# Optimization experiments

Measured on AMD Instinct MI355X. Metric: run time of the kernel, lower is better.

## Reference

```python
import jax, jax.numpy as jnp
import numpy as np

N, H, W = 2, 96, 96
HL, WL = 48, 48
NCLS = 59


def _bn_params(key, c):
    k1, k2, k3, k4 = jax.random.split(key, 4)
    g = jax.random.uniform(k1, (c,), minval=0.5, maxval=1.5)
    b = jax.random.normal(k2, (c,)) * 0.1
    m = jax.random.normal(k3, (c,)) * 0.1
    v = jax.random.uniform(k4, (c,), minval=0.5, maxval=1.5)
    return jnp.stack([g, b, m, v])  # [4, C]


def _conv_w(key, shape):
    fan_in = shape[1] * shape[2] * shape[3]
    return jax.random.normal(key, shape) / np.sqrt(fan_in)


def setup_inputs() -> dict:
    key = jax.random.key(0)
    ks = jax.random.split(key, 32)
    return {
        "c1": jax.random.normal(ks[0], (N, 256, H, W)),
        "c2": jax.random.normal(ks[1], (N, 512, HL, WL)),
        "x": jax.random.normal(ks[2], (N, 2048, HL, WL)),
        "w_r1": _conv_w(ks[3], (64, 256, 3, 3)), "bn_r1": _bn_params(ks[4], 64),
        "w_r2": _conv_w(ks[5], (64, 64, 3, 3)), "bn_r2": _bn_params(ks[6], 64),
        "w_r3": _conv_w(ks[7], (64, 512, 1, 1)), "bn_r3": _bn_params(ks[8], 64),
        "w_p1": _conv_w(ks[9], (512, 2048, 1, 1)), "bn_p1": _bn_params(ks[10], 512),
        "w_p2": _conv_w(ks[11], (512, 2048, 1, 1)), "bn_p2": _bn_params(ks[12], 512),
        "w_p3": _conv_w(ks[13], (512, 2048, 1, 1)), "bn_p3": _bn_params(ks[14], 512),
        "w_p4": _conv_w(ks[15], (512, 2048, 1, 1)), "bn_p4": _bn_params(ks[16], 512),
        "w_c5": _conv_w(ks[17], (512, 4096, 3, 3)), "bn_c5": _bn_params(ks[18], 512),
        "w_c6": _conv_w(ks[19], (NCLS, 512, 1, 1)),
        "b_c6": jax.random.normal(ks[20], (NCLS,)) * 0.01,
    }


def conv2d(x, w, padding=0, dilation=1):
    return jax.lax.conv_general_dilated(
        x, w, window_strides=(1, 1), padding=[(padding, padding)] * 2,
        rhs_dilation=(dilation, dilation),
        dimension_numbers=("NCHW", "OIHW", "NCHW"))


def bn(x, p, eps=1e-5):
    g, b, m, v = p[0], p[1], p[2], p[3]
    scale = g * jax.lax.rsqrt(v + eps)
    return (x - m[None, :, None, None]) * scale[None, :, None, None] + b[None, :, None, None]


def resize_bilinear_ac(x, oh, ow):
    # bilinear, align_corners=True (matches torch interpolate)
    n, c, h, w = x.shape
    def coords(inp, out):
        if inp == 1 or out == 1:
            return jnp.zeros((out,), jnp.float32)
        return jnp.arange(out, dtype=jnp.float32) * ((inp - 1) / (out - 1))
    ys, xs = coords(h, oh), coords(w, ow)
    y0 = jnp.clip(jnp.floor(ys).astype(jnp.int32), 0, h - 1)
    y1 = jnp.clip(y0 + 1, 0, h - 1)
    wy = (ys - y0)[None, None, :, None]
    x0 = jnp.clip(jnp.floor(xs).astype(jnp.int32), 0, w - 1)
    x1 = jnp.clip(x0 + 1, 0, w - 1)
    wx = (xs - x0)[None, None, :]
    g = x[:, :, y0, :] * (1.0 - wy) + x[:, :, y1, :] * wy  # [n,c,oh,w]
    return g[:, :, :, x0] * (1.0 - wx[:, None]) + g[:, :, :, x1] * wx[:, None]


def unfold3x3_d2(x):
    # torch unfold(kernel=3, dilation=2, padding=2, stride=1) -> [n,c,9,h*w]
    n, c, h, w = x.shape
    p = jnp.pad(x, ((0, 0), (0, 0), (2, 2), (2, 2)))
    pats = jnp.stack([p[:, :, dy:dy + h, dx:dx + w]
                      for dy in (0, 2, 4) for dx in (0, 2, 4)], axis=2)
    return pats.reshape(n, c, 9, h * w)


def adaptive_avg_pool(x, s):
    n, c, h, w = x.shape  # h, w divisible by s here
    return x.reshape(n, c, s, h // s, s, w // s).mean(axis=(3, 5))


def reference(c1, c2, x, w_r1, bn_r1, w_r2, bn_r2, w_r3, bn_r3,
              w_p1, bn_p1, w_p2, bn_p2, w_p3, bn_p3, w_p4, bn_p4,
              w_c5, bn_c5, w_c6, b_c6):
    n, _, h, w = c1.shape
    # refine(c1): two dilated 3x3 convs -> query features [n,64,h,w]
    r = jax.nn.relu(bn(conv2d(c1, w_r1, padding=2, dilation=2), bn_r1))
    r = jax.nn.relu(bn(conv2d(r, w_r2, padding=2, dilation=2), bn_r2))
    # c2 -> upsample -> refine2 (1x1) -> key features [n,64,h,w]
    c2u = resize_bilinear_ac(c2, h, w)
    c2r = jax.nn.relu(bn(conv2d(c2u, w_r3), bn_r3))
    uc2 = unfold3x3_d2(c2r)                       # [n,64,9,hw]
    q = r.reshape(n, 64, h * w)                   # [n,64,hw]
    energy = jnp.einsum("ncp,nckp->npk", q, uc2)  # [n,hw,9]
    att = jax.nn.softmax(energy, axis=-1)
    # conv5 = PyramidPooling + 3x3 conv(4096->512) + BN + ReLU
    xh, xw = x.shape[2], x.shape[3]
    feats = [x]
    for s, wp, bnp in ((1, w_p1, bn_p1), (2, w_p2, bn_p2), (3, w_p3, bn_p3), (6, w_p4, bn_p4)):
        p = jax.nn.relu(bn(conv2d(adaptive_avg_pool(x, s), wp), bnp))
        feats.append(resize_bilinear_ac(p, xh, xw))
    psp = jnp.concatenate(feats, axis=1)          # [n,4096,xh,xw]
    out = jax.nn.relu(bn(conv2d(psp, w_c5, padding=1, dilation=1), bn_c5))  # [n,512,xh,xw]
    out0 = resize_bilinear_ac(out, h, w)          # [n,512,h,w]
    uo = unfold3x3_d2(out0)                       # [n,512,9,hw]
    agg = jnp.einsum("npk,nckp->ncp", att, uo).reshape(n, 512, h, w)
    # conv6: Dropout2d in eval mode = identity, then 1x1 conv with bias
    return conv2d(agg, w_c6) + b_c6[None, :, None, None]
```

## Files before the change

### kernel.cpp

```cpp
#include <hip/hip_runtime.h>
#include <hip/hip_bf16.h>
#include <cstddef>
#include <cstdint>

typedef __hip_bfloat16 hbf;
typedef __bf16 bf16x8 __attribute__((ext_vector_type(8)));
typedef float f32x4 __attribute__((ext_vector_type(4)));

#define GLDS(gp, lp) __builtin_amdgcn_global_load_lds( \
    (const __attribute__((address_space(1))) void*)(gp), \
    (__attribute__((address_space(3))) void*)(lp), 16, 0, 0)

__device__ __forceinline__ void bn_coef(const float* __restrict__ p, int C, int c,
                                        float& s, float& t) {
    float g = p[c];
    float b = p[C + c];
    float m = p[2 * C + c];
    float v = p[3 * C + c];
    s = g * rsqrtf(v + 1e-5f);
    t = b - m * s;
}

__global__ void k_fill0(uint32_t* __restrict__ p, int n) {
    int i = blockIdx.x * blockDim.x + threadIdx.x;
    if (i < n) p[i] = 0u;
}

__global__ __launch_bounds__(256) void k_c1trans(const float* __restrict__ x,
                                                 hbf* __restrict__ c1t) {
    __shared__ float tbuf[32][33];
    const int p0 = blockIdx.x * 32, c0 = blockIdx.y * 32, n = blockIdx.z;
    const int tx = threadIdx.x, ty = threadIdx.y;
#pragma unroll
    for (int i = 0; i < 4; ++i) {
        int ci = c0 + ty * 4 + i;
        tbuf[ty * 4 + i][tx] = x[((size_t)(n * 256 + ci)) * 9216 + p0 + tx];
    }
    __syncthreads();
#pragma unroll
    for (int i = 0; i < 4; ++i) {
        int p = p0 + ty * 4 + i;
        int pp = (p / 96 + 2) * 100 + (p % 96) + 2;
        c1t[((size_t)(n * 10000 + pp)) * 256 + c0 + tx] = __float2bfloat16(tbuf[tx][ty * 4 + i]);
    }
}

template <int CI>
__global__ __launch_bounds__(256) void k_wtrans_small(const float* __restrict__ w,
                                                      hbf* __restrict__ wt) {
    int idx = blockIdx.x * 256 + threadIdx.x;
    int co = idx / CI, ci = idx % CI;
    const float* s = w + ((size_t)(co * CI + ci)) * 9;
#pragma unroll
    for (int tap = 0; tap < 9; ++tap)
        wt[((size_t)(tap * 64 + co)) * CI + ci] = __float2bfloat16(s[tap]);
}

template <int CI>
__global__ __launch_bounds__(256) void k_dconv_mfma(const hbf* __restrict__ wt,
                                                    const hbf* __restrict__ it,
                                                    float* __restrict__ accout) {
    __shared__ hbf As[3][64 * 32];
    __shared__ hbf Bs[72 * 32];
    const int tid = threadIdx.x;
    const int l = tid & 63, w = tid >> 6;
    const int P0 = blockIdx.x * 64;
    const int g  = blockIdx.y;
    const int r0 = tid >> 2;
    const int swzk = ((tid & 3) ^ (r0 & 3)) * 8;

    const int n_i = P0 / 9216;
    const int pl0 = P0 - n_i * 9216;
    const int pp0 = (pl0 / 96 + 2) * 100 + (pl0 % 96) + 2;
    const ptrdiff_t browbase = (ptrdiff_t)n_i * 10000 + pp0 + (g - 1) * 200 - 2;

    const int wn = w * 16;
    const int pl_lane = pl0 + wn + (l & 15);
    const int jb = ((pl_lane / 96 + 2) * 100 + (pl_lane % 96) + 2) - pp0;
    const int slotA = ((l >> 4) ^ (l & 3)) * 8;

    f32x4 acc[4];
#pragma unroll
    for (int i = 0; i < 4; ++i) acc[i] = {0.f, 0.f, 0.f, 0.f};

    const hbf* gA = wt + ((size_t)(g * 192 + r0)) * CI + swzk;
    const hbf* gB = it + (size_t)(browbase + r0) * CI + swzk;
    hbf* ldsA = (hbf*)As[0] + w * 512;
    hbf* ldsB = Bs + w * 512;

    for (int k0 = 0; k0 < CI; k0 += 32) {
        __syncthreads();
#pragma unroll
        for (int t = 0; t < 3; ++t)
            GLDS(gA + (size_t)t * 64 * CI + k0, ldsA + t * 2048);
        GLDS(gB + k0, ldsB);
        if (tid < 32)
            GLDS(gB + (size_t)64 * CI + k0, Bs + 2048);
        __syncthreads();
#pragma unroll
        for (int t = 0; t < 3; ++t) {
            const int brow = jb + 2 * t;
            bf16x8 bfr = *(const bf16x8*)(Bs + brow * 32 + (((l >> 4) ^ (brow & 3)) * 8));
#pragma unroll
            for (int ti = 0; ti < 4; ++ti) {
                bf16x8 af = *(const bf16x8*)(&As[t][(ti * 16 + (l & 15)) * 32 + slotA]);
                acc[ti] = __builtin_amdgcn_mfma_f32_16x16x32_bf16(af, bfr, acc[ti], 0, 0, 0);
            }
        }
    }
    const int px = P0 + wn + (l & 15);
    const int n2 = px / 9216, pl2 = px % 9216;
#pragma unroll
    for (int ti = 0; ti < 4; ++ti) {
        const int mrow = ti * 16 + (l >> 4) * 4;
        float* dst = accout + ((size_t)(n2 * 64 + mrow)) * 9216 + pl2;
#pragma unroll
        for (int r = 0; r < 4; ++r)
            atomicAdd(dst + (size_t)r * 9216, acc[ti][r]);
    }
}

__global__ __launch_bounds__(256) void k_ep_r1(const float* __restrict__ acc,
                                               const float* __restrict__ bnp,
                                               hbf* __restrict__ r1t) {
    __shared__ float ss[64], st[64];
    if (threadIdx.x < 64) {
        float s, t; bn_coef(bnp, 64, threadIdx.x, s, t);
        ss[threadIdx.x] = s; st[threadIdx.x] = t;
    }
    __syncthreads();
    const int pi = blockIdx.x * 256 + threadIdx.x;
    const int n = pi / 9216, pl = pi % 9216;
    const int pp = (pl / 96 + 2) * 100 + (pl % 96) + 2;
    hbf* dst = r1t + ((size_t)(n * 10000 + pp)) * 64;
    const float* src = acc + (size_t)n * 64 * 9216 + pl;
#pragma unroll
    for (int co = 0; co < 64; ++co)
        dst[co] = __float2bfloat16(fmaxf(fmaf(src[(size_t)co * 9216], ss[co], st[co]), 0.f));
}

__global__ void k_ep_q(const float* __restrict__ acc, const float* __restrict__ bnp,
                       float* __restrict__ q) {
    int idx = blockIdx.x * blockDim.x + threadIdx.x;
    int c = (idx / 9216) & 63;
    float s, t; bn_coef(bnp, 64, c, s, t);
    q[idx] = fmaxf(fmaf(acc[idx], s, t), 0.f);
}

__global__ __launch_bounds__(192) void k_conv1x1_c2(const float* __restrict__ c2,
                                                    const float* __restrict__ w,
                                                    float* __restrict__ outacc) {
    const int x = threadIdx.x;
    const int y = blockIdx.y * 4 + threadIdx.y;
    const int n = blockIdx.z >> 2;
    const int ci0 = (blockIdx.z & 3) * 128;
    const int cg = blockIdx.x;
    const int p = y * 48 + x;
    float acc[4];
#pragma unroll
    for (int j = 0; j < 4; ++j) acc[j] = 0.f;
    for (int ci = ci0; ci < ci0 + 128; ++ci) {
        float iv = c2[(size_t)(n * 512 + ci) * 2304 + p];
#pragma unroll
        for (int j = 0; j < 4; ++j)
            acc[j] = fmaf(iv, w[(size_t)(cg * 4 + j) * 512 + ci], acc[j]);
    }
#pragma unroll
    for (int j = 0; j < 4; ++j)
        atomicAdd(&outacc[(size_t)(n * 64 + cg * 4 + j) * 2304 + p], acc[j]);
}

__global__ void k_up96(const float* __restrict__ src, float* __restrict__ dst,
                       int C, const float* __restrict__ bnp) {
    int idx = blockIdx.x * blockDim.x + threadIdx.x;
    int p = idx % 9216;
    int nc = idx / 9216;
    int c = nc % C;
    int y = p / 96, x = p % 96;
    int yn = y * 47, xn = x * 47;
    int y0 = yn / 95, x0 = xn / 95;
    float wy = (float)(yn - y0 * 95) * (1.f / 95.f);
    float wx = (float)(xn - x0 * 95) * (1.f / 95.f);
    int y1 = min(y0 + 1, 47), x1 = min(x0 + 1, 47);
    const float* sp = src + (size_t)nc * 2304;
    float v00 = sp[y0 * 48 + x0], v01 = sp[y0 * 48 + x1];
    float v10 = sp[y1 * 48 + x0], v11 = sp[y1 * 48 + x1];
    float v = (v00 * (1.f - wx) + v01 * wx) * (1.f - wy)
            + (v10 * (1.f - wx) + v11 * wx) * wy;
    if (bnp) {
        float s, t; bn_coef(bnp, C, c, s, t);
        v = fmaxf(fmaf(v, s, t), 0.f);
    }
    dst[idx] = v;
}

__global__ __launch_bounds__(128) void k_attention(const float* __restrict__ q,
                                                   const float* __restrict__ kf,
                                                   float* __restrict__ att) {
    int tid = blockIdx.x * 128 + threadIdx.x;
    int n = tid / 9216, p = tid % 9216;
    int y = p / 96, x = p % 96;
    float qv[64];
    const float* qb = q + (size_t)n * 64 * 9216 + p;
#pragma unroll
    for (int c = 0; c < 64; ++c) qv[c] = qb[(size_t)c * 9216];
    float e[9];
    const float* kb = kf + (size_t)n * 64 * 9216;
#pragma unroll
    for (int ky = 0; ky < 3; ++ky)
#pragma unroll
        for (int kx = 0; kx < 3; ++kx) {
            int yy = y + 2 * ky - 2, xx = x + 2 * kx - 2;
            float s = 0.f;
            if (yy >= 0 && yy < 96 && xx >= 0 && xx < 96) {
                const float* kp = kb + yy * 96 + xx;
#pragma unroll
                for (int c = 0; c < 64; ++c) s = fmaf(qv[c], kp[(size_t)c * 9216], s);
            }
            e[ky * 3 + kx] = s;
        }
    float m = e[0];
#pragma unroll
    for (int k = 1; k < 9; ++k) m = fmaxf(m, e[k]);
    float sum = 0.f;
#pragma unroll
    for (int k = 0; k < 9; ++k) { e[k] = __expf(e[k] - m); sum += e[k]; }
    float inv = 1.f / sum;
    float* ap = att + (size_t)tid * 9;
#pragma unroll
    for (int k = 0; k < 9; ++k) ap[k] = e[k] * inv;
}

__global__ __launch_bounds__(64) void k_pool(const float* __restrict__ xin,
                                             float* __restrict__ pooled) {
    int b = blockIdx.x;
    int t = threadIdx.x;
    __shared__ float cells[50];
    if (t < 50) cells[t] = 0.f;
    __syncthreads();
    float rs = 0.f;
    if (t < 48) {
        const float* row = xin + (size_t)b * 2304 + t * 48;
        float s6[6];
#pragma unroll
        for (int j = 0; j < 6; ++j) {
            float s = 0.f;
#pragma unroll
            for (int i = 0; i < 8; ++i) s += row[j * 8 + i];
            s6[j] = s;
        }
        float s3a = s6[0] + s6[1], s3b = s6[2] + s6[3], s3c = s6[4] + s6[5];
        float s2a = s3a + s6[2], s2b = s6[3] + s3c;
        rs = s2a + s2b;
        int r6 = t >> 3, r3 = t >> 4, r2 = t / 24;
        atomicAdd(&cells[14 + r6 * 6 + 0], s6[0]);
        atomicAdd(&cells[14 + r6 * 6 + 1], s6[1]);
        atomicAdd(&cells[14 + r6 * 6 + 2], s6[2]);
        atomicAdd(&cells[14 + r6 * 6 + 3], s6[3]);
        atomicAdd(&cells[14 + r6 * 6 + 4], s6[4]);
        atomicAdd(&cells[14 + r6 * 6 + 5], s6[5]);
        atomicAdd(&cells[5 + r3 * 3 + 0], s3a);
        atomicAdd(&cells[5 + r3 * 3 + 1], s3b);
        atomicAdd(&cells[5 + r3 * 3 + 2], s3c);
        atomicAdd(&cells[1 + r2 * 2 + 0], s2a);
        atomicAdd(&cells[1 + r2 * 2 + 1], s2b);
    }
#pragma unroll
    for (int off = 32; off > 0; off >>= 1) rs += __shfl_down(rs, off);
    if (t == 0) atomicAdd(&cells[0], rs);
    __syncthreads();
    if (t < 50) {
        float inv = (t == 0) ? (1.f / 2304.f)
                  : (t < 5)  ? (1.f / 576.f)
                  : (t < 14) ? (1.f / 256.f)
                             : (1.f / 64.f);
        pooled[(size_t)b * 50 + t] = cells[t] * inv;
    }
}

__global__ __launch_bounds__(64) void k_pconv2(const float* __restrict__ pooled,
        const float* __restrict__ wp1, const float* __restrict__ bn1,
        const float* __restrict__ wp2, const float* __restrict__ bn2,
        const float* __restrict__ wp3, const float* __restrict__ bn3,
        const float* __restrict__ wp4, const float* __restrict__ bn4,
        float* __restrict__ pconv) {
    const int co = blockIdx.x, n = blockIdx.y;
    const int t = threadIdx.x;
    const int cell = (t < 50) ? t : 49;
    const float* w; const float* bnp;
    if (cell == 0)      { w = wp1; bnp = bn1; }
    else if (cell < 5)  { w = wp2; bnp = bn2; }
    else if (cell < 14) { w = wp3; bnp = bn3; }
    else                { w = wp4; bnp = bn4; }
    const float* pin = pooled + (size_t)n * 2048 * 50 + cell;
    const float* wr = w + (size_t)co * 2048;
    float a0 = 0.f, a1 = 0.f, a2 = 0.f, a3 = 0.f;
    for (int c = 0; c < 2048; c += 4) {
        a0 = fmaf(pin[(size_t)c * 50],       wr[c],     a0);
        a1 = fmaf(pin[(size_t)(c + 1) * 50], wr[c + 1], a1);
        a2 = fmaf(pin[(size_t)(c + 2) * 50], wr[c + 2], a2);
        a3 = fmaf(pin[(size_t)(c + 3) * 50], wr[c + 3], a3);
    }
    float a = (a0 + a1) + (a2 + a3);
    float s, tt; bn_coef(bnp, 512, co, s, tt);
    if (t < 50)
        pconv[((size_t)n * 512 + co) * 50 + cell] = fmaxf(fmaf(a, s, tt), 0.f);
}

__global__ __launch_bounds__(256) void k_wpsp_trans(const float* __restrict__ w5,
                                                    hbf* __restrict__ wpsp) {
    const int co = blockIdx.x * 64 + (threadIdx.x & 63);
    const int b = blockIdx.y;
    const int c0 = blockIdx.z * 64 + (threadIdx.x >> 6) * 16;
    for (int i = 0; i < 16; ++i) {
        int c = c0 + i;
        const float* s = w5 + ((size_t)co * 4096 + 2048 + b * 512 + c) * 9;
#pragma unroll
        for (int tap = 0; tap < 9; ++tap)
            wpsp[(((size_t)(tap * 4 + b) * 512) + c) * 512 + co] = __float2bfloat16(s[tap]);
    }
}

__global__ __launch_bounds__(64) void k_computeM2(const hbf* __restrict__ wpsp,
                                                  const float* __restrict__ pconv,
                                                  float* __restrict__ M) {
    const int cog = blockIdx.x, tap = blockIdx.y;
    const int n = blockIdx.z / 7, chunk = blockIdx.z % 7;
    const int cell0_t[7] = {0, 1, 5, 14, 23, 32, 41};
    const int ncell_t[7] = {1, 4, 9, 9, 9, 9, 9};
    const int btab[7]    = {0, 1, 2, 3, 3, 3, 3};
    const int cell0 = cell0_t[chunk], nc = ncell_t[chunk], b = btab[chunk];
    const int co = cog * 64 + threadIdx.x;
    const hbf* wb = wpsp + ((size_t)(tap * 4 + b) * 512) * 512 + co;
    const float* pc = pconv + (size_t)n * 512 * 50 + cell0;
    float acc[9];
#pragma unroll
    for (int j = 0; j < 9; ++j) acc[j] = 0.f;
    for (int c = 0; c < 512; ++c) {
        float w = __bfloat162float(wb[(size_t)c * 512]);
#pragma unroll
        for (int j = 0; j < 9; ++j)
            acc[j] = fmaf(w, pc[c * 50 + j], acc[j]);
    }
    float* Mp = M + ((size_t)(n * 512 + co) * 9 + tap) * 50 + cell0;
    for (int j = 0; j < nc; ++j) Mp[j] = acc[j];
}

struct B4 { int c0, c1, c2, c3; float w0, w1, w2, w3; };
__device__ __forceinline__ B4 cell_interp(int yy, int xx, int s, int base) {
    int sm1 = s - 1;
    int yn = yy * sm1, xn = xx * sm1;
    int y0 = yn / 47, x0 = xn / 47;
    float wy = (float)(yn - y0 * 47) * (1.f / 47.f);
    float wx = (float)(xn - x0 * 47) * (1.f / 47.f);
    int y1 = min(y0 + 1, sm1), x1 = min(x0 + 1, sm1);
    B4 r;
    r.c0 = base + y0 * s + x0; r.c1 = base + y0 * s + x1;
    r.c2 = base + y1 * s + x0; r.c3 = base + y1 * s + x1;
    r.w0 = (1.f - wy) * (1.f - wx); r.w1 = (1.f - wy) * wx;
    r.w2 = wy * (1.f - wx);         r.w3 = wy * wx;
    return r;
}

__global__ __launch_bounds__(256) void k_xtrans(const float* __restrict__ x,
                                                hbf* __restrict__ xtp) {
    __shared__ float tbuf[32][33];
    const int p0 = blockIdx.x * 32, c0 = blockIdx.y * 32, n = blockIdx.z;
    const int tx = threadIdx.x, ty = threadIdx.y;
#pragma unroll
    for (int i = 0; i < 4; ++i) {
        int ci = c0 + ty * 4 + i;
        tbuf[ty * 4 + i][tx] = x[((size_t)(n * 2048 + ci)) * 2304 + p0 + tx];
    }
    __syncthreads();
#pragma unroll
    for (int i = 0; i < 4; ++i) {
        int p = p0 + ty * 4 + i;
        int pp = (p / 48 + 1) * 50 + (p % 48) + 1;
        xtp[((size_t)(n * 2500 + pp)) * 2048 + c0 + tx] = __float2bfloat16(tbuf[tx][ty * 4 + i]);
    }
}

__global__ __launch_bounds__(256) void k_wtrans(const float* __restrict__ w5,
                                                hbf* __restrict__ wt) {
    int idx = blockIdx.x * 256 + threadIdx.x;
    int co = idx >> 11, ci = idx & 2047;
    const float* s = w5 + ((size_t)co * 4096 + ci) * 9;
#pragma unroll
    for (int tap = 0; tap < 9; ++tap)
        wt[((size_t)(tap * 512 + co)) * 2048 + ci] = __float2bfloat16(s[tap]);
}

__global__ __launch_bounds__(256) void k_conv5_mfma(const hbf* __restrict__ wt,
                                                    const hbf* __restrict__ xtp,
                                                    float* __restrict__ c5acc) {
    __shared__ hbf As[3][128 * 32];
    __shared__ hbf Bs[136 * 32];
    const int tid = threadIdx.x;
    const int l = tid & 63, w = tid >> 6;
    const int m0 = blockIdx.x * 128;
    const int P0 = blockIdx.y * 128;
    const int g  = blockIdx.z >> 1;
    const int kh = blockIdx.z & 1;
    const int n_img = P0 / 2304;
    const int pbase = P0 - n_img * 2304;
    const int r0 = tid >> 2;
    const int swzk = ((tid & 3) ^ (r0 & 3)) * 8;

    const int pp0 = pbase + 2 * (pbase / 48) + 51;
    const ptrdiff_t browbase = (ptrdiff_t)n_img * 2500 + pp0 + (g - 1) * 50 - 1;

    const int wm = (w & 1) * 64, wn = (w >> 1) * 64;
    int jb[4];
#pragma unroll
    for (int tj = 0; tj < 4; ++tj) {
        int p = pbase + wn + tj * 16 + (l & 15);
        jb[tj] = p + 2 * (p / 48) + 51 - pp0;
    }
    const int slotA = ((l >> 4) ^ (l & 3)) * 8;

    f32x4 acc[4][4];
#pragma unroll
    for (int i = 0; i < 4; ++i)
#pragma unroll
        for (int j = 0; j < 4; ++j) acc[i][j] = {0.f, 0.f, 0.f, 0.f};

    const int kbase = kh * 1024;
    const hbf* gA = wt + ((size_t)(g * 1536 + m0 + r0)) * 2048 + kbase + swzk;
    const hbf* gB = xtp + (size_t)(browbase + r0) * 2048 + kbase + swzk;
    hbf* ldsA = (hbf*)As[0] + w * 512;
    hbf* ldsB = Bs + w * 512;

    for (int k0 = 0; k0 < 1024; k0 += 32) {
        __syncthreads();
#pragma unroll
        for (int t = 0; t < 3; ++t) {
            GLDS(gA + (size_t)t * 512 * 2048 + k0,             ldsA + t * 4096);
            GLDS(gA + (size_t)t * 512 * 2048 + 64 * 2048 + k0, ldsA + t * 4096 + 2048);
        }
        GLDS(gB + k0,                      ldsB);
        GLDS(gB + (size_t)64 * 2048 + k0,  ldsB + 2048);
        if (tid < 32)
            GLDS(gB + (size_t)128 * 2048 + k0, Bs + 4096);
        __syncthreads();
#pragma unroll
        for (int t = 0; t < 3; ++t) {
            bf16x8 af[4], bfr[4];
#pragma unroll
            for (int ti = 0; ti < 4; ++ti)
                af[ti] = *(const bf16x8*)(&As[t][(wm + ti * 16 + (l & 15)) * 32 + slotA]);
#pragma unroll
            for (int tj = 0; tj < 4; ++tj) {
                const int brow = jb[tj] + t;
                bfr[tj] = *(const bf16x8*)(Bs + brow * 32 + (((l >> 4) ^ (brow & 3)) * 8));
            }
#pragma unroll
            for (int ti = 0; ti < 4; ++ti)
#pragma unroll
                for (int tj = 0; tj < 4; ++tj)
                    acc[ti][tj] = __builtin_amdgcn_mfma_f32_16x16x32_bf16(
                        af[ti], bfr[tj], acc[ti][tj], 0, 0, 0);
        }
    }
#pragma unroll
    for (int ti = 0; ti < 4; ++ti) {
        const int mrow = wm + ti * 16 + (l >> 4) * 4;
#pragma unroll
        for (int tj = 0; tj < 4; ++tj) {
            const int p = pbase + wn + tj * 16 + (l & 15);
            float* dst = c5acc + ((size_t)(n_img * 512 + m0 + mrow)) * 2304 + p;
#pragma unroll
            for (int r = 0; r < 4; ++r)
                atomicAdd(dst + (size_t)r * 2304, acc[ti][tj][r]);
        }
    }
}

__global__ __launch_bounds__(256) void k_bnrelu_psp(const float* __restrict__ c5acc,
                                                    const float* __restrict__ M,
                                                    const float* __restrict__ bnp,
                                                    hbf* __restrict__ c5out) {
    const int co = blockIdx.x, n = blockIdx.y;
    __shared__ float Ms[450];
    const float* Mrow = M + ((size_t)(n * 512 + co)) * 450;
    for (int i = threadIdx.x; i < 450; i += 256) Ms[i] = Mrow[i];
    __syncthreads();
    float s, t; bn_coef(bnp, 512, co, s, t);
    const size_t base = ((size_t)(n * 512 + co)) * 2304;
#pragma unroll
    for (int i = 0; i < 9; ++i) {
        int p = threadIdx.x + i * 256;
        int y = p / 48, x = p % 48;
        float a = c5acc[base + p];
#pragma unroll
        for (int ky = 0; ky < 3; ++ky) {
            int yy = y + ky - 1;
            if (yy < 0 || yy > 47) continue;
#pragma unroll
            for (int kx = 0; kx < 3; ++kx) {
                int xx = x + kx - 1;
                if (xx < 0 || xx > 47) continue;
                const float* Mp = Ms + (ky * 3 + kx) * 50;
                float sa = Mp[0];
                B4 b2 = cell_interp(yy, xx, 2, 1);
                B4 b3 = cell_interp(yy, xx, 3, 5);
                B4 b6 = cell_interp(yy, xx, 6, 14);
                sa = fmaf(b2.w0, Mp[b2.c0], sa); sa = fmaf(b2.w1, Mp[b2.c1], sa);
                sa = fmaf(b2.w2, Mp[b2.c2], sa); sa = fmaf(b2.w3, Mp[b2.c3], sa);
                sa = fmaf(b3.w0, Mp[b3.c0], sa); sa = fmaf(b3.w1, Mp[b3.c1], sa);
                sa = fmaf(b3.w2, Mp[b3.c2], sa); sa = fmaf(b3.w3, Mp[b3.c3], sa);
                sa = fmaf(b6.w0, Mp[b6.c0], sa); sa = fmaf(b6.w1, Mp[b6.c1], sa);
                sa = fmaf(b6.w2, Mp[b6.c2], sa); sa = fmaf(b6.w3, Mp[b6.c3], sa);
                a += sa;
            }
        }
        c5out[base + p] = __float2bfloat16(fmaxf(fmaf(a, s, t), 0.f));
    }
}

__global__ __launch_bounds__(192) void k_conv6s(const hbf* __restrict__ c5o,
                                                const float* __restrict__ w,
                                                float* __restrict__ out) {
    const int x = threadIdx.x;
    const int y = blockIdx.y * 4 + threadIdx.y;
    const int n = blockIdx.z;
    const int co = blockIdx.x;
    const int p = y * 48 + x;
    const hbf* ip = c5o + (size_t)n * 512 * 2304 + p;
    const float* wr = w + (size_t)co * 512;
    float a0 = 0.f, a1 = 0.f, a2 = 0.f, a3 = 0.f;
    for (int ci = 0; ci < 512; ci += 4) {
        a0 = fmaf(__bfloat162float(ip[(size_t)ci * 2304]),       wr[ci],     a0);
        a1 = fmaf(__bfloat162float(ip[(size_t)(ci + 1) * 2304]), wr[ci + 1], a1);
        a2 = fmaf(__bfloat162float(ip[(size_t)(ci + 2) * 2304]), wr[ci + 2], a2);
        a3 = fmaf(__bfloat162float(ip[(size_t)(ci + 3) * 2304]), wr[ci + 3], a3);
    }
    out[((size_t)n * 59 + co) * 2304 + p] = (a0 + a1) + (a2 + a3);
}

__global__ void k_final(const float* __restrict__ att, const float* __restrict__ c6o,
                        const float* __restrict__ bias, float* __restrict__ out) {
    int idx = blockIdx.x * blockDim.x + threadIdx.x;
    int p = idx % 9216;
    int nc = idx / 9216;
    int cls = nc % 59, n = nc / 59;
    int y = p / 96, x = p % 96;
    const float* ar = att + ((size_t)n * 9216 + p) * 9;
    const float* cp = c6o + (size_t)nc * 9216;
    float a = bias[cls];
#pragma unroll
    for (int ky = 0; ky < 3; ++ky)
#pragma unroll
        for (int kx = 0; kx < 3; ++kx) {
            int yy = y + 2 * ky - 2, xx = x + 2 * kx - 2;
            if (yy >= 0 && yy < 96 && xx >= 0 && xx < 96)
                a = fmaf(ar[ky * 3 + kx], cp[yy * 96 + xx], a);
        }
    out[idx] = a;
}

extern "C" void kernel_launch(void* const* d_in, const int* in_sizes, int n_in,
                              void* d_out, int out_size, void* d_ws, size_t ws_size,
                              hipStream_t stream) {
    const float* c1    = (const float*)d_in[0];
    const float* c2    = (const float*)d_in[1];
    const float* xin   = (const float*)d_in[2];
    const float* w_r1  = (const float*)d_in[3];
    const float* bn_r1 = (const float*)d_in[4];
    const float* w_r2  = (const float*)d_in[5];
    const float* bn_r2 = (const float*)d_in[6];
    const float* w_r3  = (const float*)d_in[7];
    const float* bn_r3 = (const float*)d_in[8];
    const float* w_p1  = (const float*)d_in[9];
    const float* bn_p1 = (const float*)d_in[10];
    const float* w_p2  = (const float*)d_in[11];
    const float* bn_p2 = (const float*)d_in[12];
    const float* w_p3  = (const float*)d_in[13];
    const float* bn_p3 = (const float*)d_in[14];
    const float* w_p4  = (const float*)d_in[15];
    const float* bn_p4 = (const float*)d_in[16];
    const float* w_c5  = (const float*)d_in[17];
    const float* bn_c5 = (const float*)d_in[18];
    const float* w_c6  = (const float*)d_in[19];
    const float* b_c6  = (const float*)d_in[20];
    float* out = (float*)d_out;
    (void)in_sizes; (void)n_in; (void)out_size; (void)ws_size;

    char* base = (char*)d_ws;
    float* att = (float*)base;
    char*  A   = base + 663552;
    hbf*   c1t   = (hbf*)A;
    hbf*   r1t   = (hbf*)(A + 10240000);
    float* r1acc = (float*)(A + 12800000);
    float* qacc  = (float*)(A + 17518592);
    float* c2acc = (float*)(A + 22237184);
    float* q     = (float*)(A + 23416832);
    float* c2r   = (float*)(A + 28135424);
    hbf*   wr1t  = (hbf*)(A + 32854016);
    hbf*   wr2t  = (hbf*)(A + 33148928);
    hbf*   wpsp   = (hbf*)A;
    float* pooled = (float*)(A + 48791552);
    float* pconv  = (float*)(A + 49610752);
    float* M      = (float*)(A + 49815552);
    hbf*   xtp    = (hbf*)A;
    float* c5acc  = (float*)(A + 20480000);
    hbf*   wt     = (hbf*)(A + 29917184);
    hbf*   c5out = (hbf*)A;
    float* c6s   = (float*)(A + 4718592);
    float* c6o   = (float*)(A + 5806080);

    k_fill0<<<dim3(22868), 256, 0, stream>>>((uint32_t*)A, 5854208);
    k_c1trans<<<dim3(288, 8, 2), dim3(32, 8), 0, stream>>>(c1, c1t);
    k_wtrans_small<256><<<dim3(64), 256, 0, stream>>>(w_r1, wr1t);
    k_wtrans_small<64><<<dim3(16), 256, 0, stream>>>(w_r2, wr2t);
    k_dconv_mfma<256><<<dim3(288, 3), 256, 0, stream>>>(wr1t, c1t, r1acc);
    k_ep_r1<<<dim3(72), 256, 0, stream>>>(r1acc, bn_r1, r1t);
    k_dconv_mfma<64><<<dim3(288, 3), 256, 0, stream>>>(wr2t, r1t, qacc);
    k_ep_q<<<dim3(4608), 256, 0, stream>>>(qacc, bn_r2, q);
    k_conv1x1_c2<<<dim3(16, 12, 8), dim3(48, 4), 0, stream>>>(c2, w_r3, c2acc);
    k_up96<<<dim3(2 * 64 * 9216 / 256), 256, 0, stream>>>(c2acc, c2r, 64, bn_r3);
    k_attention<<<dim3(144), 128, 0, stream>>>(q, c2r, att);
    k_pool<<<dim3(4096), 64, 0, stream>>>(xin, pooled);
    k_pconv2<<<dim3(512, 2), 64, 0, stream>>>(pooled, w_p1, bn_p1, w_p2, bn_p2,
                                              w_p3, bn_p3, w_p4, bn_p4, pconv);
    k_wpsp_trans<<<dim3(8, 4, 8), 256, 0, stream>>>(w_c5, wpsp);
    k_computeM2<<<dim3(8, 9, 14), 64, 0, stream>>>(wpsp, pconv, M);
    k_fill0<<<dim3(29216), 256, 0, stream>>>((uint32_t*)xtp, 7479296);
    k_xtrans<<<dim3(72, 64, 2), dim3(32, 8), 0, stream>>>(xin, xtp);
    k_wtrans<<<dim3(4096), 256, 0, stream>>>(w_c5, wt);
    k_conv5_mfma<<<dim3(4, 36, 6), 256, 0, stream>>>(wt, xtp, c5acc);
    k_bnrelu_psp<<<dim3(512, 2), 256, 0, stream>>>(c5acc, M, bn_c5, c5out);
    k_conv6s<<<dim3(59, 12, 2), dim3(48, 4), 0, stream>>>(c5out, w_c6, c6s);
    k_up96<<<dim3(2 * 59 * 9216 / 256), 256, 0, stream>>>(c6s, c6o, 59, nullptr);
    k_final<<<dim3(2 * 59 * 9216 / 256), 256, 0, stream>>>(att, c6o, b_c6, out);
}
```

Baseline: 791.5 us.

## Double-buffer LDS staging in MFMA convs and drop conv5 K-split

```diff
diff --git a/kernel.cpp b/kernel.cpp
--- a/kernel.cpp
+++ b/kernel.cpp
@@ -60,8 +60,8 @@
 __global__ __launch_bounds__(256) void k_dconv_mfma(const hbf* __restrict__ wt,
                                                     const hbf* __restrict__ it,
                                                     float* __restrict__ accout) {
-    __shared__ hbf As[3][64 * 32];
-    __shared__ hbf Bs[72 * 32];
+    __shared__ hbf As[2][3][64 * 32];
+    __shared__ hbf Bs[2][72 * 32];
     const int tid = threadIdx.x;
     const int l = tid & 63, w = tid >> 6;
     const int P0 = blockIdx.x * 64;
@@ -85,29 +85,39 @@
 
     const hbf* gA = wt + ((size_t)(g * 192 + r0)) * CI + swzk;
     const hbf* gB = it + (size_t)(browbase + r0) * CI + swzk;
-    hbf* ldsA = (hbf*)As[0] + w * 512;
-    hbf* ldsB = Bs + w * 512;
-
+
+#define STAGE_D(buf, k0) do {                                                  \
+        hbf* ldsA_ = &As[buf][0][0] + w * 512;                                 \
+        hbf* ldsB_ = &Bs[buf][0] + w * 512;                                    \
+        _Pragma("unroll")                                                      \
+        for (int t_ = 0; t_ < 3; ++t_)                                         \
+            GLDS(gA + (size_t)t_ * 64 * CI + (k0), ldsA_ + t_ * 2048);         \
+        GLDS(gB + (k0), ldsB_);                                                \
+        if (tid < 32)                                                          \
+            GLDS(gB + (size_t)64 * CI + (k0), &Bs[buf][0] + 2048);             \
+    } while (0)
+
+    STAGE_D(0, 0);
+    __syncthreads();
+    int cur = 0;
+#pragma unroll 2
     for (int k0 = 0; k0 < CI; k0 += 32) {
-        __syncthreads();
-#pragma unroll
-        for (int t = 0; t < 3; ++t)
-            GLDS(gA + (size_t)t * 64 * CI + k0, ldsA + t * 2048);
-        GLDS(gB + k0, ldsB);
-        if (tid < 32)
-            GLDS(gB + (size_t)64 * CI + k0, Bs + 2048);
-        __syncthreads();
+        if (k0 + 32 < CI) STAGE_D(cur ^ 1, k0 + 32);
 #pragma unroll
         for (int t = 0; t < 3; ++t) {
             const int brow = jb + 2 * t;
-            bf16x8 bfr = *(const bf16x8*)(Bs + brow * 32 + (((l >> 4) ^ (brow & 3)) * 8));
+            bf16x8 bfr = *(const bf16x8*)(&Bs[cur][0] + brow * 32 + (((l >> 4) ^ (brow & 3)) * 8));
 #pragma unroll
             for (int ti = 0; ti < 4; ++ti) {
-                bf16x8 af = *(const bf16x8*)(&As[t][(ti * 16 + (l & 15)) * 32 + slotA]);
+                bf16x8 af = *(const bf16x8*)(&As[cur][t][(ti * 16 + (l & 15)) * 32 + slotA]);
                 acc[ti] = __builtin_amdgcn_mfma_f32_16x16x32_bf16(af, bfr, acc[ti], 0, 0, 0);
             }
         }
-    }
+        __syncthreads();
+        cur ^= 1;
+    }
+#undef STAGE_D
+
     const int px = P0 + wn + (l & 15);
     const int n2 = px / 9216, pl2 = px % 9216;
 #pragma unroll
@@ -394,14 +404,13 @@
 __global__ __launch_bounds__(256) void k_conv5_mfma(const hbf* __restrict__ wt,
                                                     const hbf* __restrict__ xtp,
                                                     float* __restrict__ c5acc) {
-    __shared__ hbf As[3][128 * 32];
-    __shared__ hbf Bs[136 * 32];
+    __shared__ hbf As[2][3][128 * 32];
+    __shared__ hbf Bs[2][136 * 32];
     const int tid = threadIdx.x;
     const int l = tid & 63, w = tid >> 6;
     const int m0 = blockIdx.x * 128;
     const int P0 = blockIdx.y * 128;
-    const int g  = blockIdx.z >> 1;
-    const int kh = blockIdx.z & 1;
+    const int g  = blockIdx.z;
     const int n_img = P0 / 2304;
     const int pbase = P0 - n_img * 2304;
     const int r0 = tid >> 2;
@@ -425,34 +434,39 @@
 #pragma unroll
         for (int j = 0; j < 4; ++j) acc[i][j] = {0.f, 0.f, 0.f, 0.f};
 
-    const int kbase = kh * 1024;
-    const hbf* gA = wt + ((size_t)(g * 1536 + m0 + r0)) * 2048 + kbase + swzk;
-    const hbf* gB = xtp + (size_t)(browbase + r0) * 2048 + kbase + swzk;
-    hbf* ldsA = (hbf*)As[0] + w * 512;
-    hbf* ldsB = Bs + w * 512;
-
-    for (int k0 = 0; k0 < 1024; k0 += 32) {
-        __syncthreads();
-#pragma unroll
-        for (int t = 0; t < 3; ++t) {
-            GLDS(gA + (size_t)t * 512 * 2048 + k0,             ldsA + t * 4096);
-            GLDS(gA + (size_t)t * 512 * 2048 + 64 * 2048 + k0, ldsA + t * 4096 + 2048);
-        }
-        GLDS(gB + k0,                      ldsB);
-        GLDS(gB + (size_t)64 * 2048 + k0,  ldsB + 2048);
-        if (tid < 32)
-            GLDS(gB + (size_t)128 * 2048 + k0, Bs + 4096);
-        __syncthreads();
+    const hbf* gA = wt + ((size_t)(g * 1536 + m0 + r0)) * 2048 + swzk;
+    const hbf* gB = xtp + (size_t)(browbase + r0) * 2048 + swzk;
+
+#define STAGE5(buf, k0) do {                                                       \
+        hbf* ldsA_ = &As[buf][0][0] + w * 512;                                     \
+        hbf* ldsB_ = &Bs[buf][0] + w * 512;                                        \
+        _Pragma("unroll")                                                          \
+        for (int t_ = 0; t_ < 3; ++t_) {                                           \
+            GLDS(gA + (size_t)t_ * 512 * 2048 + (k0),             ldsA_ + t_ * 4096);      \
+            GLDS(gA + (size_t)t_ * 512 * 2048 + 64 * 2048 + (k0), ldsA_ + t_ * 4096 + 2048); \
+        }                                                                          \
+        GLDS(gB + (k0),                      ldsB_);                               \
+        GLDS(gB + (size_t)64 * 2048 + (k0),  ldsB_ + 2048);                        \
+        if (tid < 32)                                                              \
+            GLDS(gB + (size_t)128 * 2048 + (k0), &Bs[buf][0] + 4096);              \
+    } while (0)
+
+    STAGE5(0, 0);
+    __syncthreads();
+    int cur = 0;
+#pragma unroll 2
+    for (int k0 = 0; k0 < 2048; k0 += 32) {
+        if (k0 + 32 < 2048) STAGE5(cur ^ 1, k0 + 32);
 #pragma unroll
         for (int t = 0; t < 3; ++t) {
             bf16x8 af[4], bfr[4];
 #pragma unroll
             for (int ti = 0; ti < 4; ++ti)
-                af[ti] = *(const bf16x8*)(&As[t][(wm + ti * 16 + (l & 15)) * 32 + slotA]);
+                af[ti] = *(const bf16x8*)(&As[cur][t][(wm + ti * 16 + (l & 15)) * 32 + slotA]);
 #pragma unroll
             for (int tj = 0; tj < 4; ++tj) {
                 const int brow = jb[tj] + t;
-                bfr[tj] = *(const bf16x8*)(Bs + brow * 32 + (((l >> 4) ^ (brow & 3)) * 8));
+                bfr[tj] = *(const bf16x8*)(&Bs[cur][0] + brow * 32 + (((l >> 4) ^ (brow & 3)) * 8));
             }
 #pragma unroll
             for (int ti = 0; ti < 4; ++ti)
@@ -461,7 +475,11 @@
                     acc[ti][tj] = __builtin_amdgcn_mfma_f32_16x16x32_bf16(
                         af[ti], bfr[tj], acc[ti][tj], 0, 0, 0);
         }
-    }
+        __syncthreads();
+        cur ^= 1;
+    }
+#undef STAGE5
+
 #pragma unroll
     for (int ti = 0; ti < 4; ++ti) {
         const int mrow = wm + ti * 16 + (l >> 4) * 4;
@@ -628,7 +646,7 @@
     k_fill0<<<dim3(29216), 256, 0, stream>>>((uint32_t*)xtp, 7479296);
     k_xtrans<<<dim3(72, 64, 2), dim3(32, 8), 0, stream>>>(xin, xtp);
     k_wtrans<<<dim3(4096), 256, 0, stream>>>(w_c5, wt);
-    k_conv5_mfma<<<dim3(4, 36, 6), 256, 0, stream>>>(wt, xtp, c5acc);
+    k_conv5_mfma<<<dim3(4, 36, 3), 256, 0, stream>>>(wt, xtp, c5acc);
     k_bnrelu_psp<<<dim3(512, 2), 256, 0, stream>>>(c5acc, M, bn_c5, c5out);
     k_conv6s<<<dim3(59, 12, 2), dim3(48, 4), 0, stream>>>(c5out, w_c6, c6s);
     k_up96<<<dim3(2 * 59 * 9216 / 256), 256, 0, stream>>>(c6s, c6o, 59, nullptr);
```

New measurement: 743.6 us. 6.0% less time.
